# Kernel optimization log

Hardware: AMD Instinct MI355X
Metric: run time of the kernel (lower is better)

Reference implementation:

```python
import jax, jax.numpy as jnp
import numpy as np

B, H, W, C = 32, 512, 512, 3
OUT_H, OUT_W = 224, 224


def setup_inputs() -> dict:
    key = jax.random.key(0)
    k1, k2 = jax.random.split(key)
    images = jax.random.uniform(k1, (B, H, W, C), dtype=jnp.float32)
    identity = jnp.array([[1.0, 0.0, 0.0], [0.0, 1.0, 0.0]], dtype=jnp.float32)
    matrices = identity[None] + 0.05 * jax.random.normal(k2, (B, 2, 3), dtype=jnp.float32)
    return {"images": images, "matrices": matrices}


def _affine_warp(image, M):
    # image: (H, W, C); M: (2, 3) mapping output pixel (y, x, 1) -> source (y, x).
    h, w, _ = image.shape
    dt = image.dtype
    ys, xs = jnp.meshgrid(jnp.arange(h, dtype=dt), jnp.arange(w, dtype=dt), indexing="ij")
    src_y = M[0, 0] * ys + M[0, 1] * xs + M[0, 2]
    src_x = M[1, 0] * ys + M[1, 1] * xs + M[1, 2]
    y0 = jnp.floor(src_y)
    x0 = jnp.floor(src_x)
    wy = (src_y - y0)[..., None]
    wx = (src_x - x0)[..., None]
    y0i = y0.astype(jnp.int32)
    x0i = x0.astype(jnp.int32)

    def gather(yi, xi):
        valid = (yi >= 0) & (yi < h) & (xi >= 0) & (xi < w)
        yc = jnp.clip(yi, 0, h - 1)
        xc = jnp.clip(xi, 0, w - 1)
        return image[yc, xc] * valid[..., None].astype(dt)  # zero fill outside

    v00 = gather(y0i, x0i)
    v01 = gather(y0i, x0i + 1)
    v10 = gather(y0i + 1, x0i)
    v11 = gather(y0i + 1, x0i + 1)
    top = v00 * (1.0 - wx) + v01 * wx
    bot = v10 * (1.0 - wx) + v11 * wx
    return top * (1.0 - wy) + bot * wy


def reference(images, matrices):
    # batch_transform: per-sample affine warp (bilinear sampling, zero padding)
    warped = jax.vmap(_affine_warp)(images, matrices)  # (B, H, W, C)
    # batch_resize: bilinear resize to the layer's target shape
    b, _, _, c = warped.shape
    return jax.image.resize(warped, (b, OUT_H, OUT_W, c), method="bilinear")
```

## Files before the change

### kernel.cpp

```cpp
#include <hip/hip_runtime.h>
#include <math.h>

constexpr int B  = 32;
constexpr int H  = 512;
constexpr int W  = 512;
constexpr int C  = 3;
constexpr int OH = 224;
constexpr int OW = 224;

constexpr int TILE = 16;
constexpr int WIN  = 40;
constexpr int NT   = OH / TILE;

__global__ __launch_bounds__(256) void warp_resize_tiled(const float* __restrict__ img,
                                                         const float* __restrict__ mats,
                                                         float* __restrict__ out) {
    __shared__ float sW[WIN][WIN * 3];
    __shared__ float sV[TILE][WIN * 3];

    const int bid = blockIdx.x;
    const int b   = bid / (NT * NT);
    const int rm  = bid % (NT * NT);
    const int ty  = rm / NT;
    const int tx  = rm % NT;
    const int tid = threadIdx.x;

    const float* Mp = mats + b * 6;
    const float m00 = Mp[0], m01 = Mp[1], m02 = Mp[2];
    const float m10 = Mp[3], m11 = Mp[4], m12 = Mp[5];

    const float s     = 512.0f / 224.0f;
    const float invks = 224.0f / 512.0f;

    const int oy_base = ty * TILE;
    const int ox_base = tx * TILE;
    const int jy0 = (int)ceilf((oy_base + 0.5f) * s - 0.5f - s);
    const int jx0 = (int)ceilf((ox_base + 0.5f) * s - 0.5f - s);

    const float* imgb = img + (size_t)b * H * W * C;

    for (int e = tid; e < WIN * WIN; e += 256) {
        const int r = e / WIN;
        const int c = e % WIN;
        const float yf = (float)(jy0 + r);
        const float xf = (float)(jx0 + c);
        const float src_y = m00 * yf + m01 * xf + m02;
        const float src_x = m10 * yf + m11 * xf + m12;
        const float fy0 = floorf(src_y);
        const float fx0 = floorf(src_x);
        const float fy  = src_y - fy0;
        const float fx  = src_x - fx0;
        const int iy0 = (int)fy0;
        const int ix0 = (int)fx0;

        float v[4][3];
#pragma unroll
        for (int t = 0; t < 4; ++t) {
            const int yi = iy0 + (t >> 1);
            const int xi = ix0 + (t & 1);
            if (yi >= 0 && yi < H && xi >= 0 && xi < W) {
                const float* p = imgb + ((size_t)yi * W + xi) * C;
                v[t][0] = p[0]; v[t][1] = p[1]; v[t][2] = p[2];
            } else {
                v[t][0] = 0.0f; v[t][1] = 0.0f; v[t][2] = 0.0f;
            }
        }
        const float w00 = (1.0f - fy) * (1.0f - fx);
        const float w01 = (1.0f - fy) * fx;
        const float w10 = fy * (1.0f - fx);
        const float w11 = fy * fx;
        sW[r][c * 3 + 0] = v[0][0] * w00 + v[1][0] * w01 + v[2][0] * w10 + v[3][0] * w11;
        sW[r][c * 3 + 1] = v[0][1] * w00 + v[1][1] * w01 + v[2][1] * w10 + v[3][1] * w11;
        sW[r][c * 3 + 2] = v[0][2] * w00 + v[1][2] * w01 + v[2][2] * w10 + v[3][2] * w11;
    }
    __syncthreads();

    for (int e = tid; e < TILE * WIN; e += 256) {
        const int r = e / WIN;
        const int c = e % WIN;
        const int oy = oy_base + r;
        const float sfy = (oy + 0.5f) * s - 0.5f;
        const int j0 = (int)ceilf(sfy - s);
        float wk[5];
        float sum = 0.0f;
#pragma unroll
        for (int k = 0; k < 5; ++k) {
            const int jy = j0 + k;
            float wv = 1.0f - fabsf(sfy - (float)jy) * invks;
            wv = (jy >= 0 && jy < H) ? fmaxf(wv, 0.0f) : 0.0f;
            wk[k] = wv; sum += wv;
        }
        const float inv = 1.0f / sum;
        float a0 = 0.0f, a1 = 0.0f, a2 = 0.0f;
#pragma unroll
        for (int k = 0; k < 5; ++k) {
            const int rr = j0 + k - jy0;
            const float wv = wk[k];
            a0 += wv * sW[rr][c * 3 + 0];
            a1 += wv * sW[rr][c * 3 + 1];
            a2 += wv * sW[rr][c * 3 + 2];
        }
        sV[r][c * 3 + 0] = a0 * inv;
        sV[r][c * 3 + 1] = a1 * inv;
        sV[r][c * 3 + 2] = a2 * inv;
    }
    __syncthreads();

    const int oxl = tid % TILE;
    const int oyl = tid / TILE;
    const int ox  = ox_base + oxl;
    const int oy  = oy_base + oyl;
    const float sfx = (ox + 0.5f) * s - 0.5f;
    const int j0 = (int)ceilf(sfx - s);
    float wk[5];
    float sum = 0.0f;
#pragma unroll
    for (int k = 0; k < 5; ++k) {
        const int jx = j0 + k;
        float wv = 1.0f - fabsf(sfx - (float)jx) * invks;
        wv = (jx >= 0 && jx < W) ? fmaxf(wv, 0.0f) : 0.0f;
        wk[k] = wv; sum += wv;
    }
    const float inv = 1.0f / sum;
    float a0 = 0.0f, a1 = 0.0f, a2 = 0.0f;
#pragma unroll
    for (int k = 0; k < 5; ++k) {
        const int cc = j0 + k - jx0;
        const float wv = wk[k];
        a0 += wv * sV[oyl][cc * 3 + 0];
        a1 += wv * sV[oyl][cc * 3 + 1];
        a2 += wv * sV[oyl][cc * 3 + 2];
    }
    float* o = out + (((size_t)b * OH + oy) * OW + ox) * 3;
    o[0] = a0 * inv;
    o[1] = a1 * inv;
    o[2] = a2 * inv;
}

extern "C" void kernel_launch(void* const* d_in, const int* in_sizes, int n_in,
                              void* d_out, int out_size, void* d_ws, size_t ws_size,
                              hipStream_t stream) {
    const float* img  = (const float*)d_in[0];
    const float* mats = (const float*)d_in[1];
    float*       out  = (float*)d_out;

    const int blocks = B * NT * NT;
    hipLaunchKernelGGL(warp_resize_tiled, dim3(blocks), dim3(256), 0, stream, img, mats, out);
}
```

Measured before the change: 164.3 us.

## Add interior fast path, 320-thread exact loops, and XCD-aware block swizzle

```diff
diff --git a/kernel.cpp b/kernel.cpp
--- a/kernel.cpp
+++ b/kernel.cpp
@@ -11,19 +11,23 @@
 constexpr int TILE = 16;
 constexpr int WIN  = 40;
 constexpr int NT   = OH / TILE;
-
-__global__ __launch_bounds__(256) void warp_resize_tiled(const float* __restrict__ img,
-                                                         const float* __restrict__ mats,
-                                                         float* __restrict__ out) {
+constexpr int NB   = B * NT * NT;
+constexpr int THREADS = 320;
+
+__global__ __launch_bounds__(THREADS) void warp_resize_tiled(const float* __restrict__ img,
+                                                             const float* __restrict__ mats,
+                                                             float* __restrict__ out) {
     __shared__ float sW[WIN][WIN * 3];
     __shared__ float sV[TILE][WIN * 3];
 
-    const int bid = blockIdx.x;
+    int bid = (int)blockIdx.x;
+    bid = (bid & 7) * (NB / 8) + (bid >> 3);
+
     const int b   = bid / (NT * NT);
     const int rm  = bid % (NT * NT);
     const int ty  = rm / NT;
     const int tx  = rm % NT;
-    const int tid = threadIdx.x;
+    const int tid = (int)threadIdx.x;
 
     const float* Mp = mats + b * 6;
     const float m00 = Mp[0], m01 = Mp[1], m02 = Mp[2];
@@ -39,102 +43,159 @@
 
     const float* imgb = img + (size_t)b * H * W * C;
 
-    for (int e = tid; e < WIN * WIN; e += 256) {
-        const int r = e / WIN;
-        const int c = e % WIN;
-        const float yf = (float)(jy0 + r);
+    const float y_lo = (float)jy0, y_hi = (float)(jy0 + WIN - 1);
+    const float x_lo = (float)jx0, x_hi = (float)(jx0 + WIN - 1);
+    float cy00 = m00 * y_lo + m01 * x_lo + m02;
+    float cy01 = m00 * y_lo + m01 * x_hi + m02;
+    float cy10 = m00 * y_hi + m01 * x_lo + m02;
+    float cy11 = m00 * y_hi + m01 * x_hi + m02;
+    float cx00 = m10 * y_lo + m11 * x_lo + m12;
+    float cx01 = m10 * y_lo + m11 * x_hi + m12;
+    float cx10 = m10 * y_hi + m11 * x_lo + m12;
+    float cx11 = m10 * y_hi + m11 * x_hi + m12;
+    const float miny = fminf(fminf(cy00, cy01), fminf(cy10, cy11));
+    const float maxy = fmaxf(fmaxf(cy00, cy01), fmaxf(cy10, cy11));
+    const float minx = fminf(fminf(cx00, cx01), fminf(cx10, cx11));
+    const float maxx = fmaxf(fmaxf(cx00, cx01), fmaxf(cx10, cx11));
+    const bool interior = (miny >= 0.01f) && (maxy <= 510.9f) &&
+                          (minx >= 0.01f) && (maxx <= 510.9f);
+
+    {
+        const int c  = tid % WIN;
+        int       r  = tid / WIN;
         const float xf = (float)(jx0 + c);
-        const float src_y = m00 * yf + m01 * xf + m02;
-        const float src_x = m10 * yf + m11 * xf + m12;
-        const float fy0 = floorf(src_y);
-        const float fx0 = floorf(src_x);
-        const float fy  = src_y - fy0;
-        const float fx  = src_x - fx0;
-        const int iy0 = (int)fy0;
-        const int ix0 = (int)fx0;
-
-        float v[4][3];
-#pragma unroll
-        for (int t = 0; t < 4; ++t) {
-            const int yi = iy0 + (t >> 1);
-            const int xi = ix0 + (t & 1);
-            if (yi >= 0 && yi < H && xi >= 0 && xi < W) {
-                const float* p = imgb + ((size_t)yi * W + xi) * C;
-                v[t][0] = p[0]; v[t][1] = p[1]; v[t][2] = p[2];
-            } else {
-                v[t][0] = 0.0f; v[t][1] = 0.0f; v[t][2] = 0.0f;
-            }
-        }
-        const float w00 = (1.0f - fy) * (1.0f - fx);
-        const float w01 = (1.0f - fy) * fx;
-        const float w10 = fy * (1.0f - fx);
-        const float w11 = fy * fx;
-        sW[r][c * 3 + 0] = v[0][0] * w00 + v[1][0] * w01 + v[2][0] * w10 + v[3][0] * w11;
-        sW[r][c * 3 + 1] = v[0][1] * w00 + v[1][1] * w01 + v[2][1] * w10 + v[3][1] * w11;
-        sW[r][c * 3 + 2] = v[0][2] * w00 + v[1][2] * w01 + v[2][2] * w10 + v[3][2] * w11;
+        const float cY = m01 * xf + m02;
+        const float cX = m11 * xf + m12;
+
+        if (interior) {
+#pragma unroll
+            for (int it = 0; it < 5; ++it) {
+                const float yf = (float)(jy0 + r);
+                const float src_y = m00 * yf + cY;
+                const float src_x = m10 * yf + cX;
+                const float fy0 = floorf(src_y);
+                const float fx0 = floorf(src_x);
+                const float fy  = src_y - fy0;
+                const float fx  = src_x - fx0;
+                const int off = ((int)fy0 * W + (int)fx0) * 3;
+                const float* p0 = imgb + off;
+                const float* p1 = p0 + W * 3;
+                const float a0 = p0[0], a1 = p0[1], a2 = p0[2];
+                const float a3 = p0[3], a4 = p0[4], a5 = p0[5];
+                const float b0 = p1[0], b1 = p1[1], b2 = p1[2];
+                const float b3 = p1[3], b4 = p1[4], b5 = p1[5];
+                const float w00 = (1.0f - fy) * (1.0f - fx);
+                const float w01 = (1.0f - fy) * fx;
+                const float w10 = fy * (1.0f - fx);
+                const float w11 = fy * fx;
+                sW[r][c * 3 + 0] = a0 * w00 + a3 * w01 + b0 * w10 + b3 * w11;
+                sW[r][c * 3 + 1] = a1 * w00 + a4 * w01 + b1 * w10 + b4 * w11;
+                sW[r][c * 3 + 2] = a2 * w00 + a5 * w01 + b2 * w10 + b5 * w11;
+                r += 8;
+            }
+        } else {
+#pragma unroll
+            for (int it = 0; it < 5; ++it) {
+                const float yf = (float)(jy0 + r);
+                const float src_y = m00 * yf + cY;
+                const float src_x = m10 * yf + cX;
+                const float fy0 = floorf(src_y);
+                const float fx0 = floorf(src_x);
+                const float fy  = src_y - fy0;
+                const float fx  = src_x - fx0;
+                const int iy0 = (int)fy0;
+                const int ix0 = (int)fx0;
+                float v[4][3];
+#pragma unroll
+                for (int t = 0; t < 4; ++t) {
+                    const int yi = iy0 + (t >> 1);
+                    const int xi = ix0 + (t & 1);
+                    if (yi >= 0 && yi < H && xi >= 0 && xi < W) {
+                        const float* p = imgb + (yi * W + xi) * 3;
+                        v[t][0] = p[0]; v[t][1] = p[1]; v[t][2] = p[2];
+                    } else {
+                        v[t][0] = 0.0f; v[t][1] = 0.0f; v[t][2] = 0.0f;
+                    }
+                }
+                const float w00 = (1.0f - fy) * (1.0f - fx);
+                const float w01 = (1.0f - fy) * fx;
+                const float w10 = fy * (1.0f - fx);
+                const float w11 = fy * fx;
+                sW[r][c * 3 + 0] = v[0][0] * w00 + v[1][0] * w01 + v[2][0] * w10 + v[3][0] * w11;
+                sW[r][c * 3 + 1] = v[0][1] * w00 + v[1][1] * w01 + v[2][1] * w10 + v[3][1] * w11;
+                sW[r][c * 3 + 2] = v[0][2] * w00 + v[1][2] * w01 + v[2][2] * w10 + v[3][2] * w11;
+                r += 8;
+            }
+        }
     }
     __syncthreads();
 
-    for (int e = tid; e < TILE * WIN; e += 256) {
-        const int r = e / WIN;
-        const int c = e % WIN;
-        const int oy = oy_base + r;
-        const float sfy = (oy + 0.5f) * s - 0.5f;
-        const int j0 = (int)ceilf(sfy - s);
+    {
+        const int c = tid % WIN;
+        int       r = tid / WIN;
+#pragma unroll
+        for (int it = 0; it < 2; ++it) {
+            const int oy = oy_base + r;
+            const float sfy = (oy + 0.5f) * s - 0.5f;
+            const int j0 = (int)ceilf(sfy - s);
+            float wk[5];
+            float sum = 0.0f;
+#pragma unroll
+            for (int k = 0; k < 5; ++k) {
+                const int jy = j0 + k;
+                float wv = 1.0f - fabsf(sfy - (float)jy) * invks;
+                wv = (jy >= 0 && jy < H) ? fmaxf(wv, 0.0f) : 0.0f;
+                wk[k] = wv; sum += wv;
+            }
+            const float inv = 1.0f / sum;
+            float a0 = 0.0f, a1 = 0.0f, a2 = 0.0f;
+#pragma unroll
+            for (int k = 0; k < 5; ++k) {
+                const int rr = j0 + k - jy0;
+                const float wv = wk[k];
+                a0 += wv * sW[rr][c * 3 + 0];
+                a1 += wv * sW[rr][c * 3 + 1];
+                a2 += wv * sW[rr][c * 3 + 2];
+            }
+            sV[r][c * 3 + 0] = a0 * inv;
+            sV[r][c * 3 + 1] = a1 * inv;
+            sV[r][c * 3 + 2] = a2 * inv;
+            r += 8;
+        }
+    }
+    __syncthreads();
+
+    if (tid < TILE * TILE) {
+        const int oxl = tid % TILE;
+        const int oyl = tid / TILE;
+        const int ox  = ox_base + oxl;
+        const int oy  = oy_base + oyl;
+        const float sfx = (ox + 0.5f) * s - 0.5f;
+        const int j0 = (int)ceilf(sfx - s);
         float wk[5];
         float sum = 0.0f;
 #pragma unroll
         for (int k = 0; k < 5; ++k) {
-            const int jy = j0 + k;
-            float wv = 1.0f - fabsf(sfy - (float)jy) * invks;
-            wv = (jy >= 0 && jy < H) ? fmaxf(wv, 0.0f) : 0.0f;
+            const int jx = j0 + k;
+            float wv = 1.0f - fabsf(sfx - (float)jx) * invks;
+            wv = (jx >= 0 && jx < W) ? fmaxf(wv, 0.0f) : 0.0f;
             wk[k] = wv; sum += wv;
         }
         const float inv = 1.0f / sum;
         float a0 = 0.0f, a1 = 0.0f, a2 = 0.0f;
 #pragma unroll
         for (int k = 0; k < 5; ++k) {
-            const int rr = j0 + k - jy0;
+            const int cc = j0 + k - jx0;
             const float wv = wk[k];
-            a0 += wv * sW[rr][c * 3 + 0];
-            a1 += wv * sW[rr][c * 3 + 1];
-            a2 += wv * sW[rr][c * 3 + 2];
-        }
-        sV[r][c * 3 + 0] = a0 * inv;
-        sV[r][c * 3 + 1] = a1 * inv;
-        sV[r][c * 3 + 2] = a2 * inv;
+            a0 += wv * sV[oyl][cc * 3 + 0];
+            a1 += wv * sV[oyl][cc * 3 + 1];
+            a2 += wv * sV[oyl][cc * 3 + 2];
+        }
+        float* o = out + (((size_t)b * OH + oy) * OW + ox) * 3;
+        o[0] = a0 * inv;
+        o[1] = a1 * inv;
+        o[2] = a2 * inv;
     }
-    __syncthreads();
-
-    const int oxl = tid % TILE;
-    const int oyl = tid / TILE;
-    const int ox  = ox_base + oxl;
-    const int oy  = oy_base + oyl;
-    const float sfx = (ox + 0.5f) * s - 0.5f;
-    const int j0 = (int)ceilf(sfx - s);
-    float wk[5];
-    float sum = 0.0f;
-#pragma unroll
-    for (int k = 0; k < 5; ++k) {
-        const int jx = j0 + k;
-        float wv = 1.0f - fabsf(sfx - (float)jx) * invks;
-        wv = (jx >= 0 && jx < W) ? fmaxf(wv, 0.0f) : 0.0f;
-        wk[k] = wv; sum += wv;
-    }
-    const float inv = 1.0f / sum;
-    float a0 = 0.0f, a1 = 0.0f, a2 = 0.0f;
-#pragma unroll
-    for (int k = 0; k < 5; ++k) {
-        const int cc = j0 + k - jx0;
-        const float wv = wk[k];
-        a0 += wv * sV[oyl][cc * 3 + 0];
-        a1 += wv * sV[oyl][cc * 3 + 1];
-        a2 += wv * sV[oyl][cc * 3 + 2];
-    }
-    float* o = out + (((size_t)b * OH + oy) * OW + ox) * 3;
-    o[0] = a0 * inv;
-    o[1] = a1 * inv;
-    o[2] = a2 * inv;
 }
 
 extern "C" void kernel_launch(void* const* d_in, const int* in_sizes, int n_in,
@@ -144,6 +205,5 @@
     const float* mats = (const float*)d_in[1];
     float*       out  = (float*)d_out;
 
-    const int blocks = B * NT * NT;
-    hipLaunchKernelGGL(warp_resize_tiled, dim3(blocks), dim3(256), 0, stream, img, mats, out);
+    hipLaunchKernelGGL(warp_resize_tiled, dim3(NB), dim3(THREADS), 0, stream, img, mats, out);
 }
```

Measured after the change: 162.6 us. Within noise of the previous version (-1.1%).
